# Performance work log

Hardware: AMD Instinct MI355X
Metric: run time of the kernel (lower is better)

Reference implementation:

```python
import jax, jax.numpy as jnp
import numpy as np

K = 6  # hardcoded top-k in the original forward


def setup_inputs() -> dict:
    key = jax.random.key(0)
    k1, k2, k3, k4, k5 = jax.random.split(key, 5)
    N, M, C = 512, 2048, 256
    return {
        "micro": jax.random.normal(k1, (N, C), jnp.float32),
        "label": jax.random.uniform(k2, (N,), jnp.float32),
        "micro_all": jax.random.normal(k3, (M, C), jnp.float32),
        "label_all": jax.random.uniform(k4, (M,), jnp.float32),
        # fc = nn.Linear(channels, 1, bias=False) -> weight vector [C]
        "fc_w": jax.random.normal(k5, (C,), jnp.float32) * 0.05,
    }


def reference(micro, label, micro_all, label_all, fc_w):
    N, C = micro.shape
    M = micro_all.shape[0]
    # Pairwise squared differences: dis[n, m, c] = (micro_all[m,c] - micro[n,c])^2
    dis = (micro_all[None, :, :] - micro[:, None, :]) ** 2  # [N, M, C]
    # Linear(C,1,bias=False) along channel dim, minus per-pair channel mean
    anti = jnp.einsum('nmc,c->nm', dis, fc_w) - dis.mean(axis=2)  # [N, M]
    anti = jax.nn.softmax(anti, axis=1)
    # top-k mask (argsort-based selection of k largest == lax.top_k)
    _, idx = jax.lax.top_k(anti, K)  # [N, K]
    mask = jnp.zeros((N, M), anti.dtype).at[jnp.arange(N)[:, None], idx].set(1.0)
    cut = anti * mask
    cut = cut / jnp.sum(cut, axis=1, keepdims=True)  # renormalize kNN weights
    micro_tmp = micro + cut @ micro_all  # [N, C]
    # composition loss
    dis_label = jnp.abs(label_all[None, :] - label[:, None])  # [N, M]
    co_loss = jnp.asarray(1e-4, cut.dtype) + jnp.sum(dis_label * cut) / N
    return micro_tmp, co_loss
```

## Files before the change

kernel.cpp:

```cpp
#include <hip/hip_runtime.h>
#include <hip/hip_bf16.h>
#include <math.h>

#define N_Q   512
#define M_ALL 2048
#define CHN   256
#define TOPK  6
#define INV_C (1.0f / 256.0f)

#define WS_LOGIT 4096

typedef __bf16 bf16x8 __attribute__((ext_vector_type(8)));
typedef float  f32x4  __attribute__((ext_vector_type(4)));

static __device__ __forceinline__ unsigned short bfbits(float x) {
    __bf16 h = (__bf16)x;
    unsigned short u;
    __builtin_memcpy(&u, &h, 2);
    return u;
}

#define BM 64
#define BN 64
#define LDK 264

__global__ __launch_bounds__(512) void gcn_gemm(
    const float* __restrict__ micro_all,
    const float* __restrict__ micro,
    const float* __restrict__ fc_w,
    float* __restrict__ logits,
    float* __restrict__ out)
{
    __shared__ unsigned short sA[BM][LDK];
    __shared__ unsigned short sB[BN][LDK];
    __shared__ float s_bias[BM];

    const int t    = threadIdx.x;
    const int w    = t >> 6;
    const int l15  = t & 15;
    const int quad = (t >> 4) & 3;
    const int m0   = blockIdx.x * BM;
    const int n0   = blockIdx.y * BN;

    if (m0 == 0 && n0 == 0 && t == 0) out[N_Q * CHN] = 1e-4f;

    const int rg = t >> 4;
    const int c0 = (t & 15) * 4;

    float4 wv[4];
    #pragma unroll
    for (int cc = 0; cc < 4; ++cc) {
        float4 x = *(const float4*)(fc_w + c0 + cc * 64);
        x.x -= INV_C; x.y -= INV_C; x.z -= INV_C; x.w -= INV_C;
        wv[cc] = x;
    }

    #pragma unroll
    for (int i = 0; i < 2; ++i) {
        const int r = i * 32 + rg;
        const float* rp = micro_all + (size_t)(m0 + r) * CHN;
        float p = 0.0f;
        #pragma unroll
        for (int cc = 0; cc < 4; ++cc) {
            const float4 v = *(const float4*)(rp + c0 + cc * 64);
            const float sx = v.x * wv[cc].x;
            const float sy = v.y * wv[cc].y;
            const float sz = v.z * wv[cc].z;
            const float sw = v.w * wv[cc].w;
            ushort4 pk;
            pk.x = bfbits(sx); pk.y = bfbits(sy); pk.z = bfbits(sz); pk.w = bfbits(sw);
            *(ushort4*)&sA[r][c0 + cc * 64] = pk;
            p += v.x * sx + v.y * sy + v.z * sz + v.w * sw;
        }
        #pragma unroll
        for (int mask = 8; mask >= 1; mask >>= 1)
            p += __shfl_xor(p, mask, 64);
        if ((t & 15) == 0) s_bias[r] = p;
    }

    #pragma unroll
    for (int i = 0; i < 2; ++i) {
        const int r = i * 32 + rg;
        const float* rp = micro + (size_t)(n0 + r) * CHN;
        #pragma unroll
        for (int cc = 0; cc < 4; ++cc) {
            const float4 v = *(const float4*)(rp + c0 + cc * 64);
            ushort4 pk;
            pk.x = bfbits(v.x); pk.y = bfbits(v.y); pk.z = bfbits(v.z); pk.w = bfbits(v.w);
            *(ushort4*)&sB[r][c0 + cc * 64] = pk;
        }
    }
    __syncthreads();

    const int nt    = w & 3;
    const int mtp   = w >> 2;
    const int rowB  = nt * 16 + l15;
    const int rowA0 = mtp * 32 + l15;
    const int rowA1 = mtp * 32 + 16 + l15;

    f32x4 acc0 = {0.f, 0.f, 0.f, 0.f};
    f32x4 acc1 = {0.f, 0.f, 0.f, 0.f};
    #pragma unroll
    for (int ks = 0; ks < 8; ++ks) {
        const int k0 = ks * 32 + quad * 8;
        const bf16x8 a  = *(const bf16x8*)&sB[rowB][k0];
        const bf16x8 b0 = *(const bf16x8*)&sA[rowA0][k0];
        const bf16x8 b1 = *(const bf16x8*)&sA[rowA1][k0];
        acc0 = __builtin_amdgcn_mfma_f32_16x16x32_bf16(a, b0, acc0, 0, 0, 0);
        acc1 = __builtin_amdgcn_mfma_f32_16x16x32_bf16(a, b1, acc1, 0, 0, 0);
    }

    const float bias0 = s_bias[mtp * 32 + l15];
    const float bias1 = s_bias[mtp * 32 + 16 + l15];
    #pragma unroll
    for (int reg = 0; reg < 4; ++reg) {
        const int n = n0 + nt * 16 + quad * 4 + reg;
        logits[(size_t)n * M_ALL + m0 + mtp * 32 + l15]      = bias0 - 2.f * acc0[reg];
        logits[(size_t)n * M_ALL + m0 + mtp * 32 + 16 + l15] = bias1 - 2.f * acc1[reg];
    }
}

#define BLOCK 256
#define WAVES (BLOCK / 64)
#define MPT   (M_ALL / BLOCK)
#define WTOP  8
#define NCAND (WAVES * WTOP)
#define NREF  10

static __device__ __forceinline__ unsigned key_of(float f, int m) {
    unsigned u = __float_as_uint(f);
    u = (u & 0x80000000u) ? ~u : (u | 0x80000000u);
    return (u & 0xFFFFF800u) | (unsigned)m;
}

__global__ __launch_bounds__(BLOCK) void gcn_topk(
    const float* __restrict__ logits,
    const float* __restrict__ micro,
    const float* __restrict__ label,
    const float* __restrict__ micro_all,
    const float* __restrict__ label_all,
    const float* __restrict__ fc_w,
    float* __restrict__ out)
{
    __shared__ unsigned s_keys[NCAND];
    __shared__ unsigned s_top[NREF];
    __shared__ float    s_ex[NREF];

    const int n    = blockIdx.x;
    const int t    = threadIdx.x;
    const int wave = t >> 6;
    const int lane = t & 63;

    const float4 b4 = *(const float4*)(micro + (size_t)n * CHN + lane * 4);
    float4 w4 = *(const float4*)(fc_w + lane * 4);
    w4.x -= INV_C; w4.y -= INV_C; w4.z -= INV_C; w4.w -= INV_C;

    unsigned k8[MPT];
    {
        const float4 v0 = *(const float4*)(logits + (size_t)n * M_ALL + t * 8);
        const float4 v1 = *(const float4*)(logits + (size_t)n * M_ALL + t * 8 + 4);
        const int mb = t * 8;
        k8[0] = key_of(v0.x, mb + 0);
        k8[1] = key_of(v0.y, mb + 1);
        k8[2] = key_of(v0.z, mb + 2);
        k8[3] = key_of(v0.w, mb + 3);
        k8[4] = key_of(v1.x, mb + 4);
        k8[5] = key_of(v1.y, mb + 5);
        k8[6] = key_of(v1.z, mb + 6);
        k8[7] = key_of(v1.w, mb + 7);
    }

    #pragma unroll
    for (int k = 0; k < WTOP; ++k) {
        unsigned best = k8[0];
        #pragma unroll
        for (int j = 1; j < MPT; ++j) best = (k8[j] > best) ? k8[j] : best;
        #pragma unroll
        for (int mask = 32; mask > 0; mask >>= 1) {
            const unsigned ov = __shfl_xor(best, mask, 64);
            best = (ov > best) ? ov : best;
        }
        if (lane == 0) s_keys[wave * WTOP + k] = best;
        #pragma unroll
        for (int j = 0; j < MPT; ++j)
            k8[j] = (k8[j] == best) ? 0u : k8[j];
    }
    __syncthreads();

    {
        unsigned v = s_keys[lane & 31];
        #pragma unroll
        for (int k = 2; k <= 32; k <<= 1) {
            #pragma unroll
            for (int j = k >> 1; j >= 1; j >>= 1) {
                const unsigned pv = __shfl_xor(v, j, 64);
                const unsigned mx = (v > pv) ? v : pv;
                const unsigned mn = (v > pv) ? pv : v;
                const bool up    = ((lane & k) == 0);
                const bool lower = ((lane & j) == 0);
                v = (up == lower) ? mx : mn;
            }
        }
        if (wave == 0 && lane < NREF) s_top[lane] = v;
    }
    __syncthreads();

    for (int c = wave; c < NREF; c += WAVES) {
        const int m = (int)(s_top[c] & 0x7FFu);
        const float4 a = *(const float4*)(micro_all + (size_t)m * CHN + lane * 4);
        const float dx = a.x - b4.x;
        const float dy = a.y - b4.y;
        const float dz = a.z - b4.z;
        const float dw = a.w - b4.w;
        float acc = dx * dx * w4.x + dy * dy * w4.y + dz * dz * w4.z + dw * dw * w4.w;
        #pragma unroll
        for (int mask = 32; mask >= 1; mask >>= 1)
            acc += __shfl_xor(acc, mask, 64);
        if (lane == 0) s_ex[c] = acc;
    }
    __syncthreads();

    float top_val[TOPK];
    int   top_idx[TOPK];
    unsigned rtk = 0u;
    #pragma unroll
    for (int k = 0; k < TOPK; ++k) {
        float best = -INFINITY;
        int   bi   = 0;
        #pragma unroll
        for (int c = 0; c < NREF; ++c) {
            const bool avail = ((rtk >> c) & 1u) == 0u;
            const float cv = s_ex[c];
            if (avail && cv > best) { best = cv; bi = c; }
        }
        top_val[k] = best;
        top_idx[k] = (int)(s_top[bi] & 0x7FFu);
        rtk |= 1u << bi;
    }

    const float mx = top_val[0];
    float e[TOPK];
    float esum = 0.0f;
    #pragma unroll
    for (int k = 0; k < TOPK; ++k) { e[k] = __expf(top_val[k] - mx); esum += e[k]; }
    const float inv = 1.0f / esum;

    float outv = micro[(size_t)n * CHN + t];
    #pragma unroll
    for (int k = 0; k < TOPK; ++k)
        outv += (e[k] * inv) * micro_all[(size_t)top_idx[k] * CHN + t];
    out[n * CHN + t] = outv;

    if (t == 0) {
        const float lab = label[n];
        float l = 0.0f;
        #pragma unroll
        for (int k = 0; k < TOPK; ++k)
            l += (e[k] * inv) * fabsf(label_all[top_idx[k]] - lab);
        atomicAdd(out + N_Q * CHN, l * (1.0f / (float)N_Q));
    }
}

extern "C" void kernel_launch(void* const* d_in, const int* in_sizes, int n_in,
                              void* d_out, int out_size, void* d_ws, size_t ws_size,
                              hipStream_t stream) {
    const float* micro     = (const float*)d_in[0];
    const float* label     = (const float*)d_in[1];
    const float* micro_all = (const float*)d_in[2];
    const float* label_all = (const float*)d_in[3];
    const float* fc_w      = (const float*)d_in[4];
    float* out    = (float*)d_out;
    float* ws     = (float*)d_ws;
    float* logits = ws + WS_LOGIT;

    gcn_gemm<<<dim3(M_ALL / BM, N_Q / BN), 512, 0, stream>>>(
        micro_all, micro, fc_w, logits, out);
    gcn_topk<<<N_Q, BLOCK, 0, stream>>>(logits, micro, label, micro_all,
                                        label_all, fc_w, out);
}
```

Before: 80.94 us.

## Fuse logit GEMM with top-k selection, keeping logits in shared memory

The weighted micro_all operand and per-row bias now go to the workspace in a small prep kernel. A fused main kernel has each 1024-thread block compute logits for 8 query rows with MFMA into LDS, then run the top-k refinement, softmax and output per wave. This stops the full N×M logit matrix from being written to and read back from global memory. In exchange only 64 blocks are launched, each streaming the whole bf16 micro_all, and half of each MFMA tile is wasted because a 16-row fragment holds only 8 queries.

```diff
diff --git a/kernel.cpp b/kernel.cpp
--- a/kernel.cpp
+++ b/kernel.cpp
@@ -6,9 +6,11 @@
 #define M_ALL 2048
 #define CHN   256
 #define TOPK  6
+#define NREF  10
 #define INV_C (1.0f / 256.0f)
 
-#define WS_LOGIT 4096
+#define WS_AW_F   4096
+#define WS_BIAS_F (WS_AW_F + (M_ALL * CHN) / 2)
 
 typedef __bf16 bf16x8 __attribute__((ext_vector_type(8)));
 typedef float  f32x4  __attribute__((ext_vector_type(4)));
@@ -20,121 +22,45 @@
     return u;
 }
 
-#define BM 64
-#define BN 64
-#define LDK 264
-
-__global__ __launch_bounds__(512) void gcn_gemm(
-    const float* __restrict__ micro_all,
-    const float* __restrict__ micro,
-    const float* __restrict__ fc_w,
-    float* __restrict__ logits,
-    float* __restrict__ out)
-{
-    __shared__ unsigned short sA[BM][LDK];
-    __shared__ unsigned short sB[BN][LDK];
-    __shared__ float s_bias[BM];
-
-    const int t    = threadIdx.x;
-    const int w    = t >> 6;
-    const int l15  = t & 15;
-    const int quad = (t >> 4) & 3;
-    const int m0   = blockIdx.x * BM;
-    const int n0   = blockIdx.y * BN;
-
-    if (m0 == 0 && n0 == 0 && t == 0) out[N_Q * CHN] = 1e-4f;
-
-    const int rg = t >> 4;
-    const int c0 = (t & 15) * 4;
-
-    float4 wv[4];
-    #pragma unroll
-    for (int cc = 0; cc < 4; ++cc) {
-        float4 x = *(const float4*)(fc_w + c0 + cc * 64);
-        x.x -= INV_C; x.y -= INV_C; x.z -= INV_C; x.w -= INV_C;
-        wv[cc] = x;
-    }
-
-    #pragma unroll
-    for (int i = 0; i < 2; ++i) {
-        const int r = i * 32 + rg;
-        const float* rp = micro_all + (size_t)(m0 + r) * CHN;
-        float p = 0.0f;
-        #pragma unroll
-        for (int cc = 0; cc < 4; ++cc) {
-            const float4 v = *(const float4*)(rp + c0 + cc * 64);
-            const float sx = v.x * wv[cc].x;
-            const float sy = v.y * wv[cc].y;
-            const float sz = v.z * wv[cc].z;
-            const float sw = v.w * wv[cc].w;
-            ushort4 pk;
-            pk.x = bfbits(sx); pk.y = bfbits(sy); pk.z = bfbits(sz); pk.w = bfbits(sw);
-            *(ushort4*)&sA[r][c0 + cc * 64] = pk;
-            p += v.x * sx + v.y * sy + v.z * sz + v.w * sw;
-        }
-        #pragma unroll
-        for (int mask = 8; mask >= 1; mask >>= 1)
-            p += __shfl_xor(p, mask, 64);
-        if ((t & 15) == 0) s_bias[r] = p;
-    }
-
-    #pragma unroll
-    for (int i = 0; i < 2; ++i) {
-        const int r = i * 32 + rg;
-        const float* rp = micro + (size_t)(n0 + r) * CHN;
-        #pragma unroll
-        for (int cc = 0; cc < 4; ++cc) {
-            const float4 v = *(const float4*)(rp + c0 + cc * 64);
-            ushort4 pk;
-            pk.x = bfbits(v.x); pk.y = bfbits(v.y); pk.z = bfbits(v.z); pk.w = bfbits(v.w);
-            *(ushort4*)&sB[r][c0 + cc * 64] = pk;
-        }
-    }
-    __syncthreads();
-
-    const int nt    = w & 3;
-    const int mtp   = w >> 2;
-    const int rowB  = nt * 16 + l15;
-    const int rowA0 = mtp * 32 + l15;
-    const int rowA1 = mtp * 32 + 16 + l15;
-
-    f32x4 acc0 = {0.f, 0.f, 0.f, 0.f};
-    f32x4 acc1 = {0.f, 0.f, 0.f, 0.f};
-    #pragma unroll
-    for (int ks = 0; ks < 8; ++ks) {
-        const int k0 = ks * 32 + quad * 8;
-        const bf16x8 a  = *(const bf16x8*)&sB[rowB][k0];
-        const bf16x8 b0 = *(const bf16x8*)&sA[rowA0][k0];
-        const bf16x8 b1 = *(const bf16x8*)&sA[rowA1][k0];
-        acc0 = __builtin_amdgcn_mfma_f32_16x16x32_bf16(a, b0, acc0, 0, 0, 0);
-        acc1 = __builtin_amdgcn_mfma_f32_16x16x32_bf16(a, b1, acc1, 0, 0, 0);
-    }
-
-    const float bias0 = s_bias[mtp * 32 + l15];
-    const float bias1 = s_bias[mtp * 32 + 16 + l15];
-    #pragma unroll
-    for (int reg = 0; reg < 4; ++reg) {
-        const int n = n0 + nt * 16 + quad * 4 + reg;
-        logits[(size_t)n * M_ALL + m0 + mtp * 32 + l15]      = bias0 - 2.f * acc0[reg];
-        logits[(size_t)n * M_ALL + m0 + mtp * 32 + 16 + l15] = bias1 - 2.f * acc1[reg];
-    }
-}
-
-#define BLOCK 256
-#define WAVES (BLOCK / 64)
-#define MPT   (M_ALL / BLOCK)
-#define WTOP  8
-#define NCAND (WAVES * WTOP)
-#define NREF  10
-
 static __device__ __forceinline__ unsigned key_of(float f, int m) {
     unsigned u = __float_as_uint(f);
     u = (u & 0x80000000u) ? ~u : (u | 0x80000000u);
     return (u & 0xFFFFF800u) | (unsigned)m;
 }
 
-__global__ __launch_bounds__(BLOCK) void gcn_topk(
-    const float* __restrict__ logits,
+__global__ __launch_bounds__(256) void gcn_prep(
+    const float* __restrict__ micro_all,
+    const float* __restrict__ fc_w,
+    unsigned short* __restrict__ aw,
+    float* __restrict__ bias,
+    float* __restrict__ out)
+{
+    const int t    = threadIdx.x;
+    const int wave = t >> 6;
+    const int lane = t & 63;
+    const int row  = blockIdx.x * 4 + wave;
+
+    if (blockIdx.x == 0 && t == 0) out[N_Q * CHN] = 1e-4f;
+
+    const float4 a = *(const float4*)(micro_all + (size_t)row * CHN + lane * 4);
+    float4 w = *(const float4*)(fc_w + lane * 4);
+    w.x -= INV_C; w.y -= INV_C; w.z -= INV_C; w.w -= INV_C;
+
+    const float sx = a.x * w.x, sy = a.y * w.y, sz = a.z * w.z, sw = a.w * w.w;
+    ushort4 pk;
+    pk.x = bfbits(sx); pk.y = bfbits(sy); pk.z = bfbits(sz); pk.w = bfbits(sw);
+    *(ushort4*)(aw + (size_t)row * CHN + lane * 4) = pk;
+
+    float p = a.x * sx + a.y * sy + a.z * sz + a.w * sw;
+    #pragma unroll
+    for (int mask = 32; mask >= 1; mask >>= 1)
+        p += __shfl_xor(p, mask, 64);
+    if (lane == 0) bias[row] = p;
+}
+
+__global__ __launch_bounds__(1024) void gcn_main(
+    const unsigned short* __restrict__ aw,
+    const float* __restrict__ bias,
     const float* __restrict__ micro,
     const float* __restrict__ label,
     const float* __restrict__ micro_all,
@@ -142,122 +68,138 @@
     const float* __restrict__ fc_w,
     float* __restrict__ out)
 {
-    __shared__ unsigned s_keys[NCAND];
-    __shared__ unsigned s_top[NREF];
-    __shared__ float    s_ex[NREF];
-
-    const int n    = blockIdx.x;
+    __shared__ float sL[8][M_ALL + 8];
+
     const int t    = threadIdx.x;
-    const int wave = t >> 6;
+    const int w    = t >> 6;
     const int lane = t & 63;
-
-    const float4 b4 = *(const float4*)(micro + (size_t)n * CHN + lane * 4);
-    float4 w4 = *(const float4*)(fc_w + lane * 4);
-    w4.x -= INV_C; w4.y -= INV_C; w4.z -= INV_C; w4.w -= INV_C;
-
-    unsigned k8[MPT];
+    const int l15  = lane & 15;
+    const int quad = lane >> 4;
+    const int n0   = blockIdx.x * 8;
+
+    bf16x8 bfr[8];
     {
-        const float4 v0 = *(const float4*)(logits + (size_t)n * M_ALL + t * 8);
-        const float4 v1 = *(const float4*)(logits + (size_t)n * M_ALL + t * 8 + 4);
-        const int mb = t * 8;
-        k8[0] = key_of(v0.x, mb + 0);
-        k8[1] = key_of(v0.y, mb + 1);
-        k8[2] = key_of(v0.z, mb + 2);
-        k8[3] = key_of(v0.w, mb + 3);
-        k8[4] = key_of(v1.x, mb + 4);
-        k8[5] = key_of(v1.y, mb + 5);
-        k8[6] = key_of(v1.z, mb + 6);
-        k8[7] = key_of(v1.w, mb + 7);
+        const float* brow = micro + (size_t)(n0 + (l15 & 7)) * CHN;
+        #pragma unroll
+        for (int ks = 0; ks < 8; ++ks) {
+            const float4 u0 = *(const float4*)(brow + ks * 32 + quad * 8);
+            const float4 u1 = *(const float4*)(brow + ks * 32 + quad * 8 + 4);
+            bf16x8 b;
+            b[0] = (__bf16)u0.x; b[1] = (__bf16)u0.y; b[2] = (__bf16)u0.z; b[3] = (__bf16)u0.w;
+            b[4] = (__bf16)u1.x; b[5] = (__bf16)u1.y; b[6] = (__bf16)u1.z; b[7] = (__bf16)u1.w;
+            bfr[ks] = b;
+        }
     }
 
-    #pragma unroll
-    for (int k = 0; k < WTOP; ++k) {
-        unsigned best = k8[0];
-        #pragma unroll
-        for (int j = 1; j < MPT; ++j) best = (k8[j] > best) ? k8[j] : best;
-        #pragma unroll
-        for (int mask = 32; mask > 0; mask >>= 1) {
-            const unsigned ov = __shfl_xor(best, mask, 64);
-            best = (ov > best) ? ov : best;
-        }
-        if (lane == 0) s_keys[wave * WTOP + k] = best;
-        #pragma unroll
-        for (int j = 0; j < MPT; ++j)
-            k8[j] = (k8[j] == best) ? 0u : k8[j];
+    #pragma unroll 2
+    for (int si = 0; si < 8; ++si) {
+        const int s    = si * 16 + w;
+        const int mrow = s * 16 + l15;
+        const unsigned short* arow = aw + (size_t)mrow * CHN;
+
+        f32x4 acc = {0.f, 0.f, 0.f, 0.f};
+        #pragma unroll
+        for (int ks = 0; ks < 8; ++ks) {
+            const bf16x8 afr = *(const bf16x8*)(arow + ks * 32 + quad * 8);
+            acc = __builtin_amdgcn_mfma_f32_16x16x32_bf16(bfr[ks], afr, acc, 0, 0, 0);
+        }
+
+        const float bs = bias[mrow];
+        if (quad < 2) {
+            #pragma unroll
+            for (int r = 0; r < 4; ++r)
+                sL[quad * 4 + r][s * 16 + l15] = bs - 2.f * acc[r];
+        }
     }
     __syncthreads();
 
-    {
-        unsigned v = s_keys[lane & 31];
-        #pragma unroll
-        for (int k = 2; k <= 32; k <<= 1) {
-            #pragma unroll
-            for (int j = k >> 1; j >= 1; j >>= 1) {
-                const unsigned pv = __shfl_xor(v, j, 64);
-                const unsigned mx = (v > pv) ? v : pv;
-                const unsigned mn = (v > pv) ? pv : v;
-                const bool up    = ((lane & k) == 0);
-                const bool lower = ((lane & j) == 0);
-                v = (up == lower) ? mx : mn;
+    if (w < 8) {
+        const int n = n0 + w;
+
+        unsigned loc[32];
+        #pragma unroll
+        for (int j = 0; j < 32; ++j)
+            loc[j] = key_of(sL[w][j * 64 + lane], j * 64 + lane);
+
+        unsigned cand[NREF];
+        #pragma unroll
+        for (int k = 0; k < NREF; ++k) {
+            unsigned best = loc[0];
+            #pragma unroll
+            for (int j = 1; j < 32; ++j) best = (loc[j] > best) ? loc[j] : best;
+            #pragma unroll
+            for (int mask = 32; mask > 0; mask >>= 1) {
+                const unsigned ov = __shfl_xor(best, mask, 64);
+                best = (ov > best) ? ov : best;
             }
-        }
-        if (wave == 0 && lane < NREF) s_top[lane] = v;
-    }
-    __syncthreads();
-
-    for (int c = wave; c < NREF; c += WAVES) {
-        const int m = (int)(s_top[c] & 0x7FFu);
-        const float4 a = *(const float4*)(micro_all + (size_t)m * CHN + lane * 4);
-        const float dx = a.x - b4.x;
-        const float dy = a.y - b4.y;
-        const float dz = a.z - b4.z;
-        const float dw = a.w - b4.w;
-        float acc = dx * dx * w4.x + dy * dy * w4.y + dz * dz * w4.z + dw * dw * w4.w;
-        #pragma unroll
-        for (int mask = 32; mask >= 1; mask >>= 1)
-            acc += __shfl_xor(acc, mask, 64);
-        if (lane == 0) s_ex[c] = acc;
-    }
-    __syncthreads();
-
-    float top_val[TOPK];
-    int   top_idx[TOPK];
-    unsigned rtk = 0u;
-    #pragma unroll
-    for (int k = 0; k < TOPK; ++k) {
-        float best = -INFINITY;
-        int   bi   = 0;
+            cand[k] = best;
+            #pragma unroll
+            for (int j = 0; j < 32; ++j)
+                if (loc[j] == best) loc[j] = 0u;
+        }
+
+        const float4 b4 = *(const float4*)(micro + (size_t)n * CHN + lane * 4);
+        float4 w4 = *(const float4*)(fc_w + lane * 4);
+        w4.x -= INV_C; w4.y -= INV_C; w4.z -= INV_C; w4.w -= INV_C;
+
+        float ex[NREF];
         #pragma unroll
         for (int c = 0; c < NREF; ++c) {
-            const bool avail = ((rtk >> c) & 1u) == 0u;
-            const float cv = s_ex[c];
-            if (avail && cv > best) { best = cv; bi = c; }
-        }
-        top_val[k] = best;
-        top_idx[k] = (int)(s_top[bi] & 0x7FFu);
-        rtk |= 1u << bi;
-    }
-
-    const float mx = top_val[0];
-    float e[TOPK];
-    float esum = 0.0f;
-    #pragma unroll
-    for (int k = 0; k < TOPK; ++k) { e[k] = __expf(top_val[k] - mx); esum += e[k]; }
-    const float inv = 1.0f / esum;
-
-    float outv = micro[(size_t)n * CHN + t];
-    #pragma unroll
-    for (int k = 0; k < TOPK; ++k)
-        outv += (e[k] * inv) * micro_all[(size_t)top_idx[k] * CHN + t];
-    out[n * CHN + t] = outv;
-
-    if (t == 0) {
-        const float lab = label[n];
-        float l = 0.0f;
-        #pragma unroll
-        for (int k = 0; k < TOPK; ++k)
-            l += (e[k] * inv) * fabsf(label_all[top_idx[k]] - lab);
-        atomicAdd(out + N_Q * CHN, l * (1.0f / (float)N_Q));
+            const int m = (int)(cand[c] & 0x7FFu);
+            const float4 a = *(const float4*)(micro_all + (size_t)m * CHN + lane * 4);
+            const float dx = a.x - b4.x;
+            const float dy = a.y - b4.y;
+            const float dz = a.z - b4.z;
+            const float dw = a.w - b4.w;
+            float acc = dx * dx * w4.x + dy * dy * w4.y + dz * dz * w4.z + dw * dw * w4.w;
+            #pragma unroll
+            for (int mask = 32; mask >= 1; mask >>= 1)
+                acc += __shfl_xor(acc, mask, 64);
+            ex[c] = acc;
+        }
+
+        float top_val[TOPK];
+        int   top_idx[TOPK];
+        unsigned rtk = 0u;
+        #pragma unroll
+        for (int k = 0; k < TOPK; ++k) {
+            float best = -INFINITY;
+            int   bi   = 0;
+            #pragma unroll
+            for (int c = 0; c < NREF; ++c) {
+                const bool avail = ((rtk >> c) & 1u) == 0u;
+                const float cv = ex[c];
+                if (avail && cv > best) { best = cv; bi = c; }
+            }
+            top_val[k] = best;
+            top_idx[k] = (int)(cand[bi] & 0x7FFu);
+            rtk |= 1u << bi;
+        }
+
+        const float mx = top_val[0];
+        float e[TOPK];
+        float esum = 0.0f;
+        #pragma unroll
+        for (int k = 0; k < TOPK; ++k) { e[k] = __expf(top_val[k] - mx); esum += e[k]; }
+        const float inv = 1.0f / esum;
+
+        float4 o4 = b4;
+        #pragma unroll
+        for (int k = 0; k < TOPK; ++k) {
+            const float wk = e[k] * inv;
+            const float4 a = *(const float4*)(micro_all + (size_t)top_idx[k] * CHN + lane * 4);
+            o4.x += wk * a.x; o4.y += wk * a.y; o4.z += wk * a.z; o4.w += wk * a.w;
+        }
+        *(float4*)(out + (size_t)n * CHN + lane * 4) = o4;
+
+        if (lane == 0) {
+            const float lab = label[n];
+            float l = 0.0f;
+            #pragma unroll
+            for (int k = 0; k < TOPK; ++k)
+                l += (e[k] * inv) * fabsf(label_all[top_idx[k]] - lab);
+            atomicAdd(out + N_Q * CHN, l * (1.0f / (float)N_Q));
+        }
     }
 }
 
@@ -269,12 +211,12 @@
     const float* micro_all = (const float*)d_in[2];
     const float* label_all = (const float*)d_in[3];
     const float* fc_w      = (const float*)d_in[4];
-    float* out    = (float*)d_out;
-    float* ws     = (float*)d_ws;
-    float* logits = ws + WS_LOGIT;
-
-    gcn_gemm<<<dim3(M_ALL / BM, N_Q / BN), 512, 0, stream>>>(
-        micro_all, micro, fc_w, logits, out);
-    gcn_topk<<<N_Q, BLOCK, 0, stream>>>(logits, micro, label, micro_all,
-                                        label_all, fc_w, out);
-}
+    float* out  = (float*)d_out;
+    float* ws   = (float*)d_ws;
+    unsigned short* aw   = (unsigned short*)(ws + WS_AW_F);
+    float*          bias = ws + WS_BIAS_F;
+
+    gcn_prep<<<M_ALL / 4, 256, 0, stream>>>(micro_all, fc_w, aw, bias, out);
+    gcn_main<<<N_Q / 8, 1024, 0, stream>>>(aw, bias, micro, label, micro_all,
+                                           label_all, fc_w, out);
+}
```

Result: slower. 116.0 us (+43.4%).

## Split bf16 conversion into prep kernel and read operands directly from global

Applied to the files above, without the earlier changes.

Adds a prep kernel that converts micro_all (scaled by fc_w minus 1/C) and micro to bf16 once and computes per-row bias into workspace. The GEMM kernel then reads the bf16 operands straight from global memory without LDS staging or a syncthreads, using smaller 64x32 tiles and 256 threads. Before, every GEMM tile block redid the fp32 load and convert work. The cost is an extra kernel launch and a workspace round trip, plus GEMM operand loads that no longer go through shared memory.

```diff
diff --git a/kernel.cpp b/kernel.cpp
--- a/kernel.cpp
+++ b/kernel.cpp
@@ -6,9 +6,13 @@
 #define M_ALL 2048
 #define CHN   256
 #define TOPK  6
+#define NREF  10
 #define INV_C (1.0f / 256.0f)
 
-#define WS_LOGIT 4096
+#define WS_AW_F    4096
+#define WS_BIAS_F  (WS_AW_F + (M_ALL * CHN) / 2)
+#define WS_BMIC_F  (WS_BIAS_F + M_ALL)
+#define WS_LOGIT_F (WS_BMIC_F + (N_Q * CHN) / 2)
 
 typedef __bf16 bf16x8 __attribute__((ext_vector_type(8)));
 typedef float  f32x4  __attribute__((ext_vector_type(4)));
@@ -20,21 +24,61 @@
     return u;
 }
 
-#define BM 64
-#define BN 64
-#define LDK 264
-
-__global__ __launch_bounds__(512) void gcn_gemm(
+static __device__ __forceinline__ unsigned key_of(float f, int m) {
+    unsigned u = __float_as_uint(f);
+    u = (u & 0x80000000u) ? ~u : (u | 0x80000000u);
+    return (u & 0xFFFFF800u) | (unsigned)m;
+}
+
+__global__ __launch_bounds__(256) void gcn_prep(
     const float* __restrict__ micro_all,
     const float* __restrict__ micro,
     const float* __restrict__ fc_w,
-    float* __restrict__ logits,
+    unsigned short* __restrict__ aw,
+    float* __restrict__ bias,
+    unsigned short* __restrict__ bmic,
     float* __restrict__ out)
 {
-    __shared__ unsigned short sA[BM][LDK];
-    __shared__ unsigned short sB[BN][LDK];
-    __shared__ float s_bias[BM];
-
+    const int t    = threadIdx.x;
+    const int wave = t >> 6;
+    const int lane = t & 63;
+
+    if (blockIdx.x == 0 && t == 0) out[N_Q * CHN] = 1e-4f;
+
+    if (blockIdx.x < M_ALL / 4) {
+        const int row = blockIdx.x * 4 + wave;
+        const float4 a = *(const float4*)(micro_all + (size_t)row * CHN + lane * 4);
+        float4 w = *(const float4*)(fc_w + lane * 4);
+        w.x -= INV_C; w.y -= INV_C; w.z -= INV_C; w.w -= INV_C;
+
+        const float sx = a.x * w.x, sy = a.y * w.y, sz = a.z * w.z, sw = a.w * w.w;
+        ushort4 pk;
+        pk.x = bfbits(sx); pk.y = bfbits(sy); pk.z = bfbits(sz); pk.w = bfbits(sw);
+        *(ushort4*)(aw + (size_t)row * CHN + lane * 4) = pk;
+
+        float p = a.x * sx + a.y * sy + a.z * sz + a.w * sw;
+        #pragma unroll
+        for (int mask = 32; mask >= 1; mask >>= 1)
+            p += __shfl_xor(p, mask, 64);
+        if (lane == 0) bias[row] = p;
+    } else {
+        const int row = (blockIdx.x - M_ALL / 4) * 4 + wave;
+        const float4 a = *(const float4*)(micro + (size_t)row * CHN + lane * 4);
+        ushort4 pk;
+        pk.x = bfbits(a.x); pk.y = bfbits(a.y); pk.z = bfbits(a.z); pk.w = bfbits(a.w);
+        *(ushort4*)(bmic + (size_t)row * CHN + lane * 4) = pk;
+    }
+}
+
+#define BM 64
+#define BN 32
+
+__global__ __launch_bounds__(256) void gcn_gemm(
+    const unsigned short* __restrict__ aw,
+    const float* __restrict__ bias,
+    const unsigned short* __restrict__ bmic,
+    float* __restrict__ logits)
+{
     const int t    = threadIdx.x;
     const int w    = t >> 6;
     const int l15  = t & 15;
@@ -42,76 +86,27 @@
     const int m0   = blockIdx.x * BM;
     const int n0   = blockIdx.y * BN;
 
-    if (m0 == 0 && n0 == 0 && t == 0) out[N_Q * CHN] = 1e-4f;
-
-    const int rg = t >> 4;
-    const int c0 = (t & 15) * 4;
-
-    float4 wv[4];
-    #pragma unroll
-    for (int cc = 0; cc < 4; ++cc) {
-        float4 x = *(const float4*)(fc_w + c0 + cc * 64);
-        x.x -= INV_C; x.y -= INV_C; x.z -= INV_C; x.w -= INV_C;
-        wv[cc] = x;
-    }
-
-    #pragma unroll
-    for (int i = 0; i < 2; ++i) {
-        const int r = i * 32 + rg;
-        const float* rp = micro_all + (size_t)(m0 + r) * CHN;
-        float p = 0.0f;
-        #pragma unroll
-        for (int cc = 0; cc < 4; ++cc) {
-            const float4 v = *(const float4*)(rp + c0 + cc * 64);
-            const float sx = v.x * wv[cc].x;
-            const float sy = v.y * wv[cc].y;
-            const float sz = v.z * wv[cc].z;
-            const float sw = v.w * wv[cc].w;
-            ushort4 pk;
-            pk.x = bfbits(sx); pk.y = bfbits(sy); pk.z = bfbits(sz); pk.w = bfbits(sw);
-            *(ushort4*)&sA[r][c0 + cc * 64] = pk;
-            p += v.x * sx + v.y * sy + v.z * sz + v.w * sw;
-        }
-        #pragma unroll
-        for (int mask = 8; mask >= 1; mask >>= 1)
-            p += __shfl_xor(p, mask, 64);
-        if ((t & 15) == 0) s_bias[r] = p;
-    }
-
-    #pragma unroll
-    for (int i = 0; i < 2; ++i) {
-        const int r = i * 32 + rg;
-        const float* rp = micro + (size_t)(n0 + r) * CHN;
-        #pragma unroll
-        for (int cc = 0; cc < 4; ++cc) {
-            const float4 v = *(const float4*)(rp + c0 + cc * 64);
-            ushort4 pk;
-            pk.x = bfbits(v.x); pk.y = bfbits(v.y); pk.z = bfbits(v.z); pk.w = bfbits(v.w);
-            *(ushort4*)&sB[r][c0 + cc * 64] = pk;
-        }
-    }
-    __syncthreads();
-
-    const int nt    = w & 3;
-    const int mtp   = w >> 2;
-    const int rowB  = nt * 16 + l15;
-    const int rowA0 = mtp * 32 + l15;
-    const int rowA1 = mtp * 32 + 16 + l15;
+    const int nt  = w & 1;
+    const int mtp = w >> 1;
+
+    const unsigned short* brow  = bmic + (size_t)(n0 + nt * 16 + l15) * CHN;
+    const unsigned short* arow0 = aw + (size_t)(m0 + mtp * 32 + l15) * CHN;
+    const unsigned short* arow1 = arow0 + 16 * CHN;
 
     f32x4 acc0 = {0.f, 0.f, 0.f, 0.f};
     f32x4 acc1 = {0.f, 0.f, 0.f, 0.f};
     #pragma unroll
     for (int ks = 0; ks < 8; ++ks) {
         const int k0 = ks * 32 + quad * 8;
-        const bf16x8 a  = *(const bf16x8*)&sB[rowB][k0];
-        const bf16x8 b0 = *(const bf16x8*)&sA[rowA0][k0];
-        const bf16x8 b1 = *(const bf16x8*)&sA[rowA1][k0];
+        const bf16x8 a  = *(const bf16x8*)(brow + k0);
+        const bf16x8 b0 = *(const bf16x8*)(arow0 + k0);
+        const bf16x8 b1 = *(const bf16x8*)(arow1 + k0);
         acc0 = __builtin_amdgcn_mfma_f32_16x16x32_bf16(a, b0, acc0, 0, 0, 0);
         acc1 = __builtin_amdgcn_mfma_f32_16x16x32_bf16(a, b1, acc1, 0, 0, 0);
     }
 
-    const float bias0 = s_bias[mtp * 32 + l15];
-    const float bias1 = s_bias[mtp * 32 + 16 + l15];
+    const float bias0 = bias[m0 + mtp * 32 + l15];
+    const float bias1 = bias[m0 + mtp * 32 + 16 + l15];
     #pragma unroll
     for (int reg = 0; reg < 4; ++reg) {
         const int n = n0 + nt * 16 + quad * 4 + reg;
@@ -125,13 +120,6 @@
 #define MPT   (M_ALL / BLOCK)
 #define WTOP  8
 #define NCAND (WAVES * WTOP)
-#define NREF  10
-
-static __device__ __forceinline__ unsigned key_of(float f, int m) {
-    unsigned u = __float_as_uint(f);
-    u = (u & 0x80000000u) ? ~u : (u | 0x80000000u);
-    return (u & 0xFFFFF800u) | (unsigned)m;
-}
 
 __global__ __launch_bounds__(BLOCK) void gcn_topk(
     const float* __restrict__ logits,
@@ -269,12 +257,17 @@
     const float* micro_all = (const float*)d_in[2];
     const float* label_all = (const float*)d_in[3];
     const float* fc_w      = (const float*)d_in[4];
-    float* out    = (float*)d_out;
-    float* ws     = (float*)d_ws;
-    float* logits = ws + WS_LOGIT;
-
-    gcn_gemm<<<dim3(M_ALL / BM, N_Q / BN), 512, 0, stream>>>(
-        micro_all, micro, fc_w, logits, out);
+    float* out  = (float*)d_out;
+    float* ws   = (float*)d_ws;
+    unsigned short* aw     = (unsigned short*)(ws + WS_AW_F);
+    float*          bias   = ws + WS_BIAS_F;
+    unsigned short* bmic   = (unsigned short*)(ws + WS_BMIC_F);
+    float*          logits = ws + WS_LOGIT_F;
+
+    gcn_prep<<<M_ALL / 4 + N_Q / 4, 256, 0, stream>>>(
+        micro_all, micro, fc_w, aw, bias, bmic, out);
+    gcn_gemm<<<dim3(M_ALL / BM, N_Q / BN), 256, 0, stream>>>(
+        aw, bias, bmic, logits);
     gcn_topk<<<N_Q, BLOCK, 0, stream>>>(logits, micro, label, micro_all,
                                         label_all, fc_w, out);
 }
```

Measured after the change: 88.57 us. +9.4%, slower.
